# Kernel optimization log

Measured on AMD Instinct MI355X. Metric: run time of the kernel, lower is better.

Reference implementation:

```python
import jax, jax.numpy as jnp
import numpy as np

N_NODES = 524288
N_EDGES = 4194304
NUM_GRAPHS = 4096
F_IN = 4
PHI_HID = 128
PHI_OUT = 128
F_HID = 256
SCORE_DIM = 2


def _glorot(key, fan_in, fan_out):
    s = jnp.sqrt(2.0 / (fan_in + fan_out)).astype(jnp.float32)
    return jax.random.normal(key, (fan_in, fan_out), dtype=jnp.float32) * s


def setup_inputs() -> dict:
    key = jax.random.key(0)
    ks = jax.random.split(key, 16)
    x = jax.random.normal(ks[0], (N_NODES, F_IN), dtype=jnp.float32)
    edge_index = jax.random.randint(ks[1], (2, N_EDGES), 0, N_NODES, dtype=jnp.int64)
    batch = jnp.sort(jax.random.randint(ks[2], (N_NODES,), 0, NUM_GRAPHS, dtype=jnp.int64))
    # Phi MLP: in -> hid -> hid -> out (num_layers=2 hidden blocks)
    phi_w0 = _glorot(ks[3], F_IN, PHI_HID); phi_b0 = jnp.zeros((PHI_HID,), jnp.float32)
    phi_w1 = _glorot(ks[4], PHI_HID, PHI_HID); phi_b1 = jnp.zeros((PHI_HID,), jnp.float32)
    phi_w2 = _glorot(ks[5], PHI_HID, PHI_OUT); phi_b2 = jnp.zeros((PHI_OUT,), jnp.float32)
    # F MLP head: in -> hid -> hid -> score_dim
    f_w0 = _glorot(ks[6], PHI_OUT, F_HID); f_b0 = jnp.zeros((F_HID,), jnp.float32)
    f_w1 = _glorot(ks[7], F_HID, F_HID); f_b1 = jnp.zeros((F_HID,), jnp.float32)
    f_w2 = _glorot(ks[8], F_HID, SCORE_DIM); f_b2 = jnp.zeros((SCORE_DIM,), jnp.float32)
    return {"x": x, "edge_index": edge_index, "batch": batch,
            "phi_w0": phi_w0, "phi_b0": phi_b0, "phi_w1": phi_w1, "phi_b1": phi_b1,
            "phi_w2": phi_w2, "phi_b2": phi_b2,
            "f_w0": f_w0, "f_b0": f_b0, "f_w1": f_w1, "f_b1": f_b1,
            "f_w2": f_w2, "f_b2": f_b2}


def reference(x, edge_index, batch,
              phi_w0, phi_b0, phi_w1, phi_b1, phi_w2, phi_b2,
              f_w0, f_b0, f_w1, f_b1, f_w2, f_b2):
    # PhiMessagePassing.update ignores aggr_out: the scatter-add over edge_index
    # is mathematically dead. Node update = phi(x) per node.
    h = jax.nn.relu(x @ phi_w0 + phi_b0)          # [N, PHI_HID]
    h = jax.nn.relu(h @ phi_w1 + phi_b1)          # [N, PHI_HID]
    h = h @ phi_w2 + phi_b2                        # [N, PHI_OUT]
    # global_add_pool: segment sum by graph id
    g = jax.ops.segment_sum(h, batch, num_segments=NUM_GRAPHS)  # [G, PHI_OUT]
    # F head MLP
    g = jax.nn.relu(g @ f_w0 + f_b0)
    g = jax.nn.relu(g @ f_w1 + f_b1)
    out = g @ f_w2 + f_b2                          # [G, SCORE_DIM]
    return out
```

## Files before the change

### kernel.cpp

```cpp
#include <hip/hip_runtime.h>
#include <hip/hip_bf16.h>

#define NNODES   524288
#define NGRAPHS  4096
#define GS       12

typedef __attribute__((ext_vector_type(8)))  short short8;
typedef __attribute__((ext_vector_type(4)))  float f32x4;
typedef __attribute__((ext_vector_type(16))) float f32x16;

static __device__ __forceinline__ unsigned short f2bf(float f) {
    __hip_bfloat16 h = __float2bfloat16(f);
    return *reinterpret_cast<unsigned short*>(&h);
}

static __device__ __forceinline__ int swz(int node, int chunk) {
    return node * 128 + ((chunk ^ (node & 15)) << 3);
}

__global__ __launch_bounds__(256) void prep_weights(
        const float* __restrict__ w0, const float* __restrict__ w1,
        const float* __restrict__ w2,
        unsigned short* __restrict__ w0F, unsigned short* __restrict__ w1F,
        unsigned short* __restrict__ w2F) {
    int e = blockIdx.x * 256 + threadIdx.x;
    if (e < 16384) {
        const int j = e & 7, lane = (e >> 3) & 63, mt = (e >> 9) & 1,
                  ks = (e >> 10) & 7, half = (e >> 13) & 1;
        const int of = half * 64 + mt * 32 + (lane & 31);
        const int k  = ks * 16 + (lane >> 5) * 8 + j;
        w1F[e] = f2bf(w1[k * 128 + of]);
    } else if (e < 32768) {
        const int i = e - 16384;
        const int j = i & 7, lane = (i >> 3) & 63, mt = (i >> 9) & 1,
                  ks = (i >> 10) & 7, half = (i >> 13) & 1;
        const int of = half * 64 + mt * 32 + (lane & 31);
        const int k  = ks * 16 + (lane >> 5) * 8 + j;
        w2F[i] = f2bf(w2[k * 128 + of]);
    } else if (e < 34816) {
        const int i = e - 32768;
        const int j = i & 7, lane = (i >> 3) & 63, mt = (i >> 9) & 1,
                  half = (i >> 10) & 1;
        const int of = half * 64 + mt * 32 + (lane & 31);
        const int k  = (lane >> 5) * 8 + j;
        w0F[i] = (k < 4) ? f2bf(w0[k * 128 + of]) : (unsigned short)0;
    }
}

__global__ __launch_bounds__(256, 3) void phi_kernel(
        const float* __restrict__ x, const int* __restrict__ batch,
        const unsigned short* __restrict__ w0F, const float* __restrict__ b0,
        const unsigned short* __restrict__ w1F, const float* __restrict__ b1,
        const unsigned short* __restrict__ w2F, const float* __restrict__ b2,
        float* __restrict__ g) {
    __shared__ __align__(16) unsigned short hb[128 * 128];
    const int tid  = threadIdx.x;
    const int lane = tid & 63;
    const int wv   = tid >> 6;
    const int half = wv & 1;
    const int wof  = half * 64;
    const int nb   = (wv >> 1) * 64;
    const int n0   = blockIdx.x * 128;
    const int l31  = lane & 31;
    const int h    = lane >> 5;

    const int gi = batch[n0 + nb + lane];
    const int gp = __shfl_up(gi, 1);
    const unsigned long long mask = __ballot((lane == 0) || (gi != gp));

    f32x16 acc[4];

    auto writeback = [&](const float* __restrict__ bias) {
        #pragma unroll
        for (int mt = 0; mt < 2; ++mt) {
            #pragma unroll
            for (int g4 = 0; g4 < 4; ++g4) {
                const int of0 = wof + mt*32 + 8*g4 + 4*h;
                const float4 bv = *reinterpret_cast<const float4*>(bias + of0);
                #pragma unroll
                for (int nt = 0; nt < 2; ++nt) {
                    const int node = nb + nt*32 + l31;
                    const f32x16 A = acc[mt*2 + nt];
                    ushort4 s;
                    s.x = f2bf(fmaxf(A[g4*4+0] + bv.x, 0.f));
                    s.y = f2bf(fmaxf(A[g4*4+1] + bv.y, 0.f));
                    s.z = f2bf(fmaxf(A[g4*4+2] + bv.z, 0.f));
                    s.w = f2bf(fmaxf(A[g4*4+3] + bv.w, 0.f));
                    const int chunk = (wof >> 3) + mt*4 + g4;
                    *reinterpret_cast<ushort4*>(&hb[swz(node, chunk) + h*4]) = s;
                }
            }
        }
    };

    {
        short8 af[2];
        #pragma unroll
        for (int mt = 0; mt < 2; ++mt)
            af[mt] = *reinterpret_cast<const short8*>(
                w0F + ((half*2 + mt)*64 + lane)*8);
        short8 bf[2];
        #pragma unroll
        for (int nt = 0; nt < 2; ++nt) {
            const float4 xv = *reinterpret_cast<const float4*>(
                x + (size_t)(n0 + nb + nt*32 + l31) * 4);
            short8 v = (short8){0,0,0,0,0,0,0,0};
            if (h == 0) {
                v[0] = (short)f2bf(xv.x); v[1] = (short)f2bf(xv.y);
                v[2] = (short)f2bf(xv.z); v[3] = (short)f2bf(xv.w);
            }
            bf[nt] = v;
        }
        #pragma unroll
        for (int t = 0; t < 4; ++t) acc[t] = (f32x16){};
        #pragma unroll
        for (int mt = 0; mt < 2; ++mt)
            #pragma unroll
            for (int nt = 0; nt < 2; ++nt)
                acc[mt*2 + nt] = __builtin_amdgcn_mfma_f32_32x32x16_bf16(
                    af[mt], bf[nt], acc[mt*2 + nt], 0, 0, 0);
    }
    writeback(b0);
    __syncthreads();

    #pragma unroll
    for (int t = 0; t < 4; ++t) acc[t] = (f32x16){};
    #pragma unroll
    for (int ks = 0; ks < 8; ++ks) {
        short8 a[2], b[2];
        #pragma unroll
        for (int mt = 0; mt < 2; ++mt)
            a[mt] = *reinterpret_cast<const short8*>(
                w1F + (((half*8 + ks)*2 + mt)*64 + lane)*8);
        #pragma unroll
        for (int nt = 0; nt < 2; ++nt)
            b[nt] = *reinterpret_cast<const short8*>(
                &hb[swz(nb + nt*32 + l31, ks*2 + h)]);
        #pragma unroll
        for (int mt = 0; mt < 2; ++mt)
            #pragma unroll
            for (int nt = 0; nt < 2; ++nt)
                acc[mt*2 + nt] = __builtin_amdgcn_mfma_f32_32x32x16_bf16(
                    a[mt], b[nt], acc[mt*2 + nt], 0, 0, 0);
    }
    __syncthreads();
    writeback(b1);
    __syncthreads();

    #pragma unroll
    for (int t = 0; t < 4; ++t) acc[t] = (f32x16){};
    #pragma unroll
    for (int ks = 0; ks < 8; ++ks) {
        short8 a[2], bb[2];
        #pragma unroll
        for (int mtn = 0; mtn < 2; ++mtn)
            a[mtn] = *reinterpret_cast<const short8*>(
                &hb[swz(nb + mtn*32 + l31, ks*2 + h)]);
        #pragma unroll
        for (int ntc = 0; ntc < 2; ++ntc)
            bb[ntc] = *reinterpret_cast<const short8*>(
                w2F + (((half*8 + ks)*2 + ntc)*64 + lane)*8);
        #pragma unroll
        for (int mtn = 0; mtn < 2; ++mtn)
            #pragma unroll
            for (int ntc = 0; ntc < 2; ++ntc)
                acc[mtn*2 + ntc] = __builtin_amdgcn_mfma_f32_32x32x16_bf16(
                    a[mtn], bb[ntc], acc[mtn*2 + ntc], 0, 0, 0);
    }

    float b2v[2];
    #pragma unroll
    for (int ntc = 0; ntc < 2; ++ntc) b2v[ntc] = b2[wof + ntc*32 + l31];

    unsigned long long rem = mask & (mask - 1);
    int s = 0;
    while (true) {
        const int e = rem ? (int)__builtin_ctzll(rem) : 64;
        const int grun = __shfl(gi, s);
        const float cnt = (float)(e - s);
        float* gdst = g + (size_t)grun * 128 + wof;
        #pragma unroll
        for (int ntc = 0; ntc < 2; ++ntc) {
            float val = 0.f;
            #pragma unroll
            for (int mtn = 0; mtn < 2; ++mtn) {
                const f32x16 A = acc[mtn*2 + ntc];
                #pragma unroll
                for (int r = 0; r < 16; ++r) {
                    const int node = mtn*32 + (r & 3) + 8*(r >> 2) + 4*h;
                    const float inc = (node >= s && node < e) ? 1.f : 0.f;
                    val = fmaf(A[r], inc, val);
                }
            }
            val += __shfl_xor(val, 32);
            if (h == 0)
                atomicAdd(gdst + ntc*32 + l31, fmaf(cnt, b2v[ntc], val));
        }
        if (!rem) break;
        s = e;
        rem &= rem - 1;
    }
}

__global__ __launch_bounds__(256) void head_kernel(
        const float* __restrict__ g,
        const float* __restrict__ fw0, const float* __restrict__ fb0,
        const float* __restrict__ fw1, const float* __restrict__ fb1,
        const float* __restrict__ fw2, const float* __restrict__ fb2,
        float* __restrict__ out) {
    __shared__ float gS[128 * GS];
    __shared__ float h1T[256 * GS];
    __shared__ float red[4][8];
    const int tid = threadIdx.x;
    const int g0  = blockIdx.x * 4;

    {
        const int gr = tid >> 6, k0 = (tid & 63) * 2;
        const float2 v = *reinterpret_cast<const float2*>(
            g + (size_t)(g0 + gr) * 128 + k0);
        gS[(k0+0)*GS + gr] = v.x;
        gS[(k0+1)*GS + gr] = v.y;
    }
    __syncthreads();

    float a1[4];
    #pragma unroll
    for (int i = 0; i < 4; ++i) a1[i] = 0.f;
    #pragma unroll 4
    for (int k = 0; k < 128; ++k) {
        const float w = fw0[k * 256 + tid];
        const f32x4 v0 = *reinterpret_cast<const f32x4*>(&gS[k*GS]);
        #pragma unroll
        for (int j = 0; j < 4; ++j)
            a1[j] = fmaf(v0[j], w, a1[j]);
    }
    {
        const float bb = fb0[tid];
        f32x4 s0;
        #pragma unroll
        for (int j = 0; j < 4; ++j)
            s0[j] = fmaxf(a1[j] + bb, 0.f);
        *reinterpret_cast<f32x4*>(&h1T[tid*GS]) = s0;
    }
    __syncthreads();

    float a2[4];
    #pragma unroll
    for (int i = 0; i < 4; ++i) a2[i] = 0.f;
    #pragma unroll 4
    for (int k = 0; k < 256; ++k) {
        const float w = fw1[k * 256 + tid];
        const f32x4 v0 = *reinterpret_cast<const f32x4*>(&h1T[k*GS]);
        #pragma unroll
        for (int j = 0; j < 4; ++j)
            a2[j] = fmaf(v0[j], w, a2[j]);
    }

    float p[8];
    {
        const float bb  = fb1[tid];
        const float w2a = fw2[tid*2 + 0];
        const float w2b = fw2[tid*2 + 1];
        #pragma unroll
        for (int i = 0; i < 4; ++i) {
            const float h2 = fmaxf(a2[i] + bb, 0.f);
            p[i*2 + 0] = h2 * w2a;
            p[i*2 + 1] = h2 * w2b;
        }
    }
    #pragma unroll
    for (int i = 0; i < 8; ++i) {
        float v = p[i];
        v += __shfl_xor(v, 32); v += __shfl_xor(v, 16); v += __shfl_xor(v, 8);
        v += __shfl_xor(v, 4);  v += __shfl_xor(v, 2);  v += __shfl_xor(v, 1);
        p[i] = v;
    }
    if ((tid & 63) == 0) {
        #pragma unroll
        for (int i = 0; i < 8; ++i) red[tid >> 6][i] = p[i];
    }
    __syncthreads();
    if (tid < 8)
        out[g0*2 + tid] = red[0][tid] + red[1][tid] + red[2][tid] + red[3][tid]
                        + fb2[tid & 1];
}

extern "C" void kernel_launch(void* const* d_in, const int* in_sizes, int n_in,
                              void* d_out, int out_size, void* d_ws, size_t ws_size,
                              hipStream_t stream) {
    const float* x   = (const float*)d_in[0];
    const int*   batch = (const int*)d_in[2];
    const float* w0  = (const float*)d_in[3];
    const float* b0  = (const float*)d_in[4];
    const float* w1  = (const float*)d_in[5];
    const float* b1  = (const float*)d_in[6];
    const float* w2  = (const float*)d_in[7];
    const float* b2  = (const float*)d_in[8];
    const float* fw0 = (const float*)d_in[9];
    const float* fb0 = (const float*)d_in[10];
    const float* fw1 = (const float*)d_in[11];
    const float* fb1 = (const float*)d_in[12];
    const float* fw2 = (const float*)d_in[13];
    const float* fb2 = (const float*)d_in[14];
    float* out = (float*)d_out;

    float* g = (float*)d_ws;
    unsigned short* w1F = (unsigned short*)((char*)d_ws + (size_t)NGRAPHS * 128 * 4);
    unsigned short* w2F = w1F + 128 * 128;
    unsigned short* w0F = w2F + 128 * 128;

    (void)hipMemsetAsync(g, 0, (size_t)NGRAPHS * 128 * sizeof(float), stream);
    prep_weights<<<136, 256, 0, stream>>>(w0, w1, w2, w0F, w1F, w2F);
    phi_kernel<<<NNODES / 128, 256, 0, stream>>>(x, batch, w0F, b0, w1F, b1, w2F, b2, g);
    head_kernel<<<NGRAPHS / 4, 256, 0, stream>>>(g, fw0, fb0, fw1, fb1, fw2, fb2, out);
}
```

Before: 180.7 us.

## Split phi kernel across 64-node blocks with per-wave output quarters

Restructures the phi MLP kernel so each block handles 64 nodes, with each of the four waves computing one 32-feature quarter instead of a 64x64 sub-tile. Shared memory is halved and double-buffered (h1/h2), which removes one barrier, and occupancy rises to 4 blocks per SIMD. A fast path handles the common case where all 64 nodes belong to one graph. The memset of the pooled buffer is folded into the weight-prep kernel. The cost is that each wave now reloads full weight fragments per block and the number of blocks doubles, so weight traffic per node goes up.

```diff
diff --git a/kernel.cpp b/kernel.cpp
--- a/kernel.cpp
+++ b/kernel.cpp
@@ -22,88 +22,77 @@
         const float* __restrict__ w0, const float* __restrict__ w1,
         const float* __restrict__ w2,
         unsigned short* __restrict__ w0F, unsigned short* __restrict__ w1F,
-        unsigned short* __restrict__ w2F) {
-    int e = blockIdx.x * 256 + threadIdx.x;
+        unsigned short* __restrict__ w2F, float* __restrict__ g) {
+    const int e = blockIdx.x * 256 + threadIdx.x;
+    reinterpret_cast<float4*>(g)[e] = make_float4(0.f, 0.f, 0.f, 0.f);
     if (e < 16384) {
-        const int j = e & 7, lane = (e >> 3) & 63, mt = (e >> 9) & 1,
-                  ks = (e >> 10) & 7, half = (e >> 13) & 1;
-        const int of = half * 64 + mt * 32 + (lane & 31);
+        const int j = e & 7, lane = (e >> 3) & 63, ks = (e >> 9) & 7, q = (e >> 12) & 3;
+        const int of = q * 32 + (lane & 31);
         const int k  = ks * 16 + (lane >> 5) * 8 + j;
         w1F[e] = f2bf(w1[k * 128 + of]);
     } else if (e < 32768) {
         const int i = e - 16384;
-        const int j = i & 7, lane = (i >> 3) & 63, mt = (i >> 9) & 1,
-                  ks = (i >> 10) & 7, half = (i >> 13) & 1;
-        const int of = half * 64 + mt * 32 + (lane & 31);
+        const int j = i & 7, lane = (i >> 3) & 63, ks = (i >> 9) & 7, q = (i >> 12) & 3;
+        const int of = q * 32 + (lane & 31);
         const int k  = ks * 16 + (lane >> 5) * 8 + j;
         w2F[i] = f2bf(w2[k * 128 + of]);
     } else if (e < 34816) {
         const int i = e - 32768;
-        const int j = i & 7, lane = (i >> 3) & 63, mt = (i >> 9) & 1,
-                  half = (i >> 10) & 1;
-        const int of = half * 64 + mt * 32 + (lane & 31);
+        const int j = i & 7, lane = (i >> 3) & 63, q = (i >> 9) & 3;
+        const int of = q * 32 + (lane & 31);
         const int k  = (lane >> 5) * 8 + j;
         w0F[i] = (k < 4) ? f2bf(w0[k * 128 + of]) : (unsigned short)0;
     }
 }
 
-__global__ __launch_bounds__(256, 3) void phi_kernel(
+__global__ __launch_bounds__(256, 4) void phi_kernel(
         const float* __restrict__ x, const int* __restrict__ batch,
         const unsigned short* __restrict__ w0F, const float* __restrict__ b0,
         const unsigned short* __restrict__ w1F, const float* __restrict__ b1,
         const unsigned short* __restrict__ w2F, const float* __restrict__ b2,
         float* __restrict__ g) {
-    __shared__ __align__(16) unsigned short hb[128 * 128];
+    __shared__ __align__(16) unsigned short hb[2 * 64 * 128];
+    unsigned short* const h1 = hb;
+    unsigned short* const h2 = hb + 64 * 128;
     const int tid  = threadIdx.x;
     const int lane = tid & 63;
-    const int wv   = tid >> 6;
-    const int half = wv & 1;
-    const int wof  = half * 64;
-    const int nb   = (wv >> 1) * 64;
-    const int n0   = blockIdx.x * 128;
+    const int q    = tid >> 6;
+    const int n0   = blockIdx.x * 64;
     const int l31  = lane & 31;
     const int h    = lane >> 5;
 
-    const int gi = batch[n0 + nb + lane];
+    const int gi = batch[n0 + lane];
     const int gp = __shfl_up(gi, 1);
     const unsigned long long mask = __ballot((lane == 0) || (gi != gp));
 
-    f32x16 acc[4];
-
-    auto writeback = [&](const float* __restrict__ bias) {
-        #pragma unroll
-        for (int mt = 0; mt < 2; ++mt) {
+    f32x16 acc[2];
+
+    auto writeback = [&](const float* __restrict__ bias, unsigned short* __restrict__ dst) {
+        #pragma unroll
+        for (int g4 = 0; g4 < 4; ++g4) {
+            const int of0 = q*32 + 8*g4 + 4*h;
+            const float4 bv = *reinterpret_cast<const float4*>(bias + of0);
             #pragma unroll
-            for (int g4 = 0; g4 < 4; ++g4) {
-                const int of0 = wof + mt*32 + 8*g4 + 4*h;
-                const float4 bv = *reinterpret_cast<const float4*>(bias + of0);
-                #pragma unroll
-                for (int nt = 0; nt < 2; ++nt) {
-                    const int node = nb + nt*32 + l31;
-                    const f32x16 A = acc[mt*2 + nt];
-                    ushort4 s;
-                    s.x = f2bf(fmaxf(A[g4*4+0] + bv.x, 0.f));
-                    s.y = f2bf(fmaxf(A[g4*4+1] + bv.y, 0.f));
-                    s.z = f2bf(fmaxf(A[g4*4+2] + bv.z, 0.f));
-                    s.w = f2bf(fmaxf(A[g4*4+3] + bv.w, 0.f));
-                    const int chunk = (wof >> 3) + mt*4 + g4;
-                    *reinterpret_cast<ushort4*>(&hb[swz(node, chunk) + h*4]) = s;
-                }
+            for (int nt = 0; nt < 2; ++nt) {
+                const int node = nt*32 + l31;
+                const f32x16 A = acc[nt];
+                ushort4 s;
+                s.x = f2bf(fmaxf(A[g4*4+0] + bv.x, 0.f));
+                s.y = f2bf(fmaxf(A[g4*4+1] + bv.y, 0.f));
+                s.z = f2bf(fmaxf(A[g4*4+2] + bv.z, 0.f));
+                s.w = f2bf(fmaxf(A[g4*4+3] + bv.w, 0.f));
+                *reinterpret_cast<ushort4*>(&dst[swz(node, q*4 + g4) + h*4]) = s;
             }
         }
     };
 
     {
-        short8 af[2];
-        #pragma unroll
-        for (int mt = 0; mt < 2; ++mt)
-            af[mt] = *reinterpret_cast<const short8*>(
-                w0F + ((half*2 + mt)*64 + lane)*8);
+        const short8 af = *reinterpret_cast<const short8*>(w0F + (q*64 + lane)*8);
         short8 bf[2];
         #pragma unroll
         for (int nt = 0; nt < 2; ++nt) {
             const float4 xv = *reinterpret_cast<const float4*>(
-                x + (size_t)(n0 + nb + nt*32 + l31) * 4);
+                x + (size_t)(n0 + nt*32 + l31) * 4);
             short8 v = (short8){0,0,0,0,0,0,0,0};
             if (h == 0) {
                 v[0] = (short)f2bf(xv.x); v[1] = (short)f2bf(xv.y);
@@ -111,80 +100,73 @@
             }
             bf[nt] = v;
         }
-        #pragma unroll
-        for (int t = 0; t < 4; ++t) acc[t] = (f32x16){};
-        #pragma unroll
-        for (int mt = 0; mt < 2; ++mt)
-            #pragma unroll
-            for (int nt = 0; nt < 2; ++nt)
-                acc[mt*2 + nt] = __builtin_amdgcn_mfma_f32_32x32x16_bf16(
-                    af[mt], bf[nt], acc[mt*2 + nt], 0, 0, 0);
-    }
-    writeback(b0);
-    __syncthreads();
-
-    #pragma unroll
-    for (int t = 0; t < 4; ++t) acc[t] = (f32x16){};
+        acc[0] = (f32x16){}; acc[1] = (f32x16){};
+        #pragma unroll
+        for (int nt = 0; nt < 2; ++nt)
+            acc[nt] = __builtin_amdgcn_mfma_f32_32x32x16_bf16(
+                af, bf[nt], acc[nt], 0, 0, 0);
+    }
+    writeback(b0, h1);
+    __syncthreads();
+
+    acc[0] = (f32x16){}; acc[1] = (f32x16){};
     #pragma unroll
     for (int ks = 0; ks < 8; ++ks) {
-        short8 a[2], b[2];
-        #pragma unroll
-        for (int mt = 0; mt < 2; ++mt)
-            a[mt] = *reinterpret_cast<const short8*>(
-                w1F + (((half*8 + ks)*2 + mt)*64 + lane)*8);
+        const short8 a = *reinterpret_cast<const short8*>(
+            w1F + ((q*8 + ks)*64 + lane)*8);
+        short8 b[2];
         #pragma unroll
         for (int nt = 0; nt < 2; ++nt)
             b[nt] = *reinterpret_cast<const short8*>(
-                &hb[swz(nb + nt*32 + l31, ks*2 + h)]);
-        #pragma unroll
-        for (int mt = 0; mt < 2; ++mt)
-            #pragma unroll
-            for (int nt = 0; nt < 2; ++nt)
-                acc[mt*2 + nt] = __builtin_amdgcn_mfma_f32_32x32x16_bf16(
-                    a[mt], b[nt], acc[mt*2 + nt], 0, 0, 0);
-    }
-    __syncthreads();
-    writeback(b1);
-    __syncthreads();
-
-    #pragma unroll
-    for (int t = 0; t < 4; ++t) acc[t] = (f32x16){};
+                &h1[swz(nt*32 + l31, ks*2 + h)]);
+        #pragma unroll
+        for (int nt = 0; nt < 2; ++nt)
+            acc[nt] = __builtin_amdgcn_mfma_f32_32x32x16_bf16(
+                a, b[nt], acc[nt], 0, 0, 0);
+    }
+    writeback(b1, h2);
+    __syncthreads();
+
+    acc[0] = (f32x16){}; acc[1] = (f32x16){};
     #pragma unroll
     for (int ks = 0; ks < 8; ++ks) {
-        short8 a[2], bb[2];
+        short8 a[2];
         #pragma unroll
         for (int mtn = 0; mtn < 2; ++mtn)
             a[mtn] = *reinterpret_cast<const short8*>(
-                &hb[swz(nb + mtn*32 + l31, ks*2 + h)]);
-        #pragma unroll
-        for (int ntc = 0; ntc < 2; ++ntc)
-            bb[ntc] = *reinterpret_cast<const short8*>(
-                w2F + (((half*8 + ks)*2 + ntc)*64 + lane)*8);
+                &h2[swz(mtn*32 + l31, ks*2 + h)]);
+        const short8 bb = *reinterpret_cast<const short8*>(
+            w2F + ((q*8 + ks)*64 + lane)*8);
         #pragma unroll
         for (int mtn = 0; mtn < 2; ++mtn)
+            acc[mtn] = __builtin_amdgcn_mfma_f32_32x32x16_bf16(
+                a[mtn], bb, acc[mtn], 0, 0, 0);
+    }
+
+    const float b2v = b2[q*32 + l31];
+
+    if (mask == 1ull) {
+        float val = 0.f;
+        #pragma unroll
+        for (int mtn = 0; mtn < 2; ++mtn) {
+            const f32x16 A = acc[mtn];
             #pragma unroll
-            for (int ntc = 0; ntc < 2; ++ntc)
-                acc[mtn*2 + ntc] = __builtin_amdgcn_mfma_f32_32x32x16_bf16(
-                    a[mtn], bb[ntc], acc[mtn*2 + ntc], 0, 0, 0);
-    }
-
-    float b2v[2];
-    #pragma unroll
-    for (int ntc = 0; ntc < 2; ++ntc) b2v[ntc] = b2[wof + ntc*32 + l31];
-
-    unsigned long long rem = mask & (mask - 1);
-    int s = 0;
-    while (true) {
-        const int e = rem ? (int)__builtin_ctzll(rem) : 64;
-        const int grun = __shfl(gi, s);
-        const float cnt = (float)(e - s);
-        float* gdst = g + (size_t)grun * 128 + wof;
-        #pragma unroll
-        for (int ntc = 0; ntc < 2; ++ntc) {
+            for (int r = 0; r < 16; ++r) val += A[r];
+        }
+        val += __shfl_xor(val, 32);
+        if (h == 0)
+            atomicAdd(g + (size_t)gi * 128 + q*32 + l31, fmaf(64.f, b2v, val));
+    } else {
+        unsigned long long rem = mask & (mask - 1);
+        int s = 0;
+        while (true) {
+            const int e = rem ? (int)__builtin_ctzll(rem) : 64;
+            const int grun = __shfl(gi, s);
+            const float cnt = (float)(e - s);
             float val = 0.f;
             #pragma unroll
             for (int mtn = 0; mtn < 2; ++mtn) {
-                const f32x16 A = acc[mtn*2 + ntc];
+                const f32x16 A = acc[mtn];
                 #pragma unroll
                 for (int r = 0; r < 16; ++r) {
                     const int node = mtn*32 + (r & 3) + 8*(r >> 2) + 4*h;
@@ -194,11 +176,11 @@
             }
             val += __shfl_xor(val, 32);
             if (h == 0)
-                atomicAdd(gdst + ntc*32 + l31, fmaf(cnt, b2v[ntc], val));
-        }
-        if (!rem) break;
-        s = e;
-        rem &= rem - 1;
+                atomicAdd(g + (size_t)grun * 128 + q*32 + l31, fmaf(cnt, b2v, val));
+            if (!rem) break;
+            s = e;
+            rem &= rem - 1;
+        }
     }
 }
 
@@ -309,8 +291,7 @@
     unsigned short* w2F = w1F + 128 * 128;
     unsigned short* w0F = w2F + 128 * 128;
 
-    (void)hipMemsetAsync(g, 0, (size_t)NGRAPHS * 128 * sizeof(float), stream);
-    prep_weights<<<136, 256, 0, stream>>>(w0, w1, w2, w0F, w1F, w2F);
-    phi_kernel<<<NNODES / 128, 256, 0, stream>>>(x, batch, w0F, b0, w1F, b1, w2F, b2, g);
+    prep_weights<<<512, 256, 0, stream>>>(w0, w1, w2, w0F, w1F, w2F, g);
+    phi_kernel<<<NNODES / 64, 256, 0, stream>>>(x, batch, w0F, b0, w1F, b1, w2F, b2, g);
     head_kernel<<<NGRAPHS / 4, 256, 0, stream>>>(g, fw0, fb0, fw1, fb1, fw2, fb2, out);
 }
```

Result: no change. 179.0 us (-0.9%).
